# Kernel tuning notes

Measured on AMD Instinct MI355X. Metric: run time of the kernel, lower is better.

## Reference

```python
import jax, jax.numpy as jnp
import numpy as np

NU, NI, E, B, D = 100000, 50000, 1000000, 250000, 64
MSG_EPS = 1e-7   # GENConv message epsilon
BN_EPS = 1e-5    # BatchNorm1d epsilon


def setup_inputs() -> dict:
    key = jax.random.key(0)
    ks = jax.random.split(key, 8)
    x_user = jax.random.normal(ks[0], (NU, D), jnp.float32)
    x_item = jax.random.normal(ks[1], (NI, D), jnp.float32)
    src_u = jax.random.randint(ks[2], (E,), 0, NU)
    dst_i = jax.random.randint(ks[3], (E,), 0, NI)
    edge_ui = jnp.stack([src_u, dst_i]).astype(jnp.int32)   # (user, rates, item)
    pu = jax.random.randint(ks[4], (B,), 0, NU)
    pi = jax.random.randint(ks[5], (B,), 0, NI)
    pred_edge = jnp.stack([pu, pi]).astype(jnp.int32)       # supervision edges
    # per-layer (3), per-edge-type (2: 0 = user->item conv, 1 = item->user conv)
    W1 = jax.random.normal(ks[6], (3, 2, D, 2 * D), jnp.float32) / np.sqrt(D).astype(np.float32)
    b1 = jnp.zeros((3, 2, 2 * D), jnp.float32)
    gamma = jnp.ones((3, 2, 2 * D), jnp.float32)
    beta = jnp.zeros((3, 2, 2 * D), jnp.float32)
    W2 = jax.random.normal(ks[7], (3, 2, 2 * D, D), jnp.float32) / np.sqrt(2 * D).astype(np.float32)
    b2 = jnp.zeros((3, 2, D), jnp.float32)
    return dict(x_user=x_user, x_item=x_item, W1=W1, b1=b1, gamma=gamma,
                beta=beta, W2=W2, b2=b2, edge_ui=edge_ui, pred_edge=pred_edge)


def _genconv(x_src, x_dst, src_idx, dst_idx, n_dst, W1, b1, g, bt, W2, b2):
    # message: relu(x_j) + eps   (no edge attrs)
    m = jax.nn.relu(x_src[src_idx]) + MSG_EPS                     # [E, D]
    # softmax aggregation over incoming edges per destination (t = 1)
    mx = jax.ops.segment_max(m, dst_idx, num_segments=n_dst)      # [N_dst, D]
    ex = jnp.exp(m - mx[dst_idx])
    den = jax.ops.segment_sum(ex, dst_idx, num_segments=n_dst)
    w = ex / den[dst_idx]
    agg = jax.ops.segment_sum(w * m, dst_idx, num_segments=n_dst) # [N_dst, D]
    # root skip + MLP([D, 2D, D]) with BatchNorm + ReLU on hidden layer
    h = agg + x_dst
    h = h @ W1 + b1                                               # [N_dst, 2D]
    mu = h.mean(axis=0)
    var = h.var(axis=0)
    h = g * (h - mu) * jax.lax.rsqrt(var + BN_EPS) + bt
    h = jax.nn.relu(h)
    return h @ W2 + b2                                            # [N_dst, D]


def reference(x_user, x_item, W1, b1, gamma, beta, W2, b2, edge_ui, pred_edge):
    u_idx, i_idx = edge_ui[0], edge_ui[1]
    xu, xi = x_user, x_item
    for l in range(3):
        # to_hetero: one conv per edge type; aggr='sum' trivial (one edge type per dst)
        new_i = _genconv(xu, xi, u_idx, i_idx, NI,
                         W1[l, 0], b1[l, 0], gamma[l, 0], beta[l, 0], W2[l, 0], b2[l, 0])
        new_u = _genconv(xi, xu, i_idx, u_idx, NU,
                         W1[l, 1], b1[l, 1], gamma[l, 1], beta[l, 1], W2[l, 1], b2[l, 1])
        xu = jax.nn.relu(new_u)
        xi = jax.nn.relu(new_i)
    # decoder: dot product on supervision edges
    return (xu[pred_edge[0]] * xi[pred_edge[1]]).sum(axis=-1)     # [B]
```

## Files before the change

### kernel.cpp

```cpp
#include <hip/hip_runtime.h>
#include <hip/hip_fp16.h>

#define NUSR 100000
#define NITM 50000
#define NEDG 1000000
#define NPRED 250000
#define DD 64
#define DD2 128
#define MSG_EPS 1e-7f
#define BN_EPS 1e-5f
#define SCAN_B 1024
#define LOG2E 1.44269504088896340736f
#define LN2F 0.69314718055994530942f

#define KI 98
#define KU 98
#define EPB 4096
#define ICAP 1536

typedef _Float16 f16x8 __attribute__((ext_vector_type(8)));
typedef float f32x4 __attribute__((ext_vector_type(4)));


__device__ __forceinline__ float exp2a(float x) {
    float r; asm("v_exp_f32 %0, %1" : "=v"(r) : "v"(x)); return r;
}

__global__ __launch_bounds__(256) void count_k(
    const int* __restrict__ u_idx, const int* __restrict__ i_idx,
    int* __restrict__ deg_u, int* __restrict__ deg_i)
{
    int base = (blockIdx.x * 256 + threadIdx.x) * 4;
    int u[4], it[4];
    #pragma unroll
    for (int q = 0; q < 4; q++) {
        int e = base + q;
        u[q]  = (e < NEDG) ? u_idx[e] : -1;
        it[q] = (e < NEDG) ? i_idx[e] : -1;
    }
    #pragma unroll
    for (int q = 0; q < 4; q++) if (it[q] >= 0) atomicAdd(&deg_i[it[q]], 1);
    #pragma unroll
    for (int q = 0; q < 4; q++) if (u[q] >= 0) atomicAdd(&deg_u[u[q]], 1);
}

__global__ __launch_bounds__(SCAN_B) void scan1_k(
    const int* __restrict__ deg_i, const int* __restrict__ deg_u,
    int* __restrict__ part_i, int* __restrict__ part_u,
    int* __restrict__ bsum_i, int* __restrict__ bsum_u, int nbi)
{
    __shared__ int s[SCAN_B];
    const int* deg; int* partial; int* bsum; int n, bb;
    if ((int)blockIdx.x < nbi) { deg = deg_i; partial = part_i; bsum = bsum_i; n = NITM; bb = blockIdx.x; }
    else { deg = deg_u; partial = part_u; bsum = bsum_u; n = NUSR; bb = blockIdx.x - nbi; }
    int tid = threadIdx.x;
    int i = bb * SCAN_B + tid;
    s[tid] = (i < n) ? deg[i] : 0;
    __syncthreads();
    for (int off = 1; off < SCAN_B; off <<= 1) {
        int t = (tid >= off) ? s[tid - off] : 0;
        __syncthreads();
        s[tid] += t;
        __syncthreads();
    }
    if (i < n) partial[i] = s[tid];
    if (tid == SCAN_B - 1) bsum[bb] = s[tid];
}

__global__ __launch_bounds__(128) void scan2_k(
    int* __restrict__ bsum_i, int* __restrict__ bsum_u, int nbi, int nbu)
{
    __shared__ int s[128];
    int* bsum = (blockIdx.x == 0) ? bsum_i : bsum_u;
    int nb = (blockIdx.x == 0) ? nbi : nbu;
    int tid = threadIdx.x;
    s[tid] = (tid < nb) ? bsum[tid] : 0;
    __syncthreads();
    for (int off = 1; off < 128; off <<= 1) {
        int t = (tid >= off) ? s[tid - off] : 0;
        __syncthreads();
        s[tid] += t;
        __syncthreads();
    }
    if (tid < nb) bsum[tid] = (tid == 0) ? 0 : s[tid - 1];
}

__global__ __launch_bounds__(SCAN_B) void scan3_k(
    const int* __restrict__ deg_i, const int* __restrict__ deg_u,
    const int* __restrict__ part_i, const int* __restrict__ part_u,
    const int* __restrict__ bsum_i, const int* __restrict__ bsum_u,
    int* __restrict__ rowptr_i, int* __restrict__ rowptr_u,
    int* __restrict__ bcur_i, int* __restrict__ bcur_u, int nbi)
{
    const int* deg; const int* partial; const int* bsum;
    int* rowptr; int* bcur; int n, bb, sh;
    if ((int)blockIdx.x < nbi) {
        deg = deg_i; partial = part_i; bsum = bsum_i;
        rowptr = rowptr_i; bcur = bcur_i; n = NITM; bb = blockIdx.x; sh = 9;
    } else {
        deg = deg_u; partial = part_u; bsum = bsum_u;
        rowptr = rowptr_u; bcur = bcur_u; n = NUSR; bb = blockIdx.x - nbi; sh = 10;
    }
    int i = bb * SCAN_B + threadIdx.x;
    if (i < n) {
        int rs = partial[i] - deg[i] + bsum[bb];
        rowptr[i] = rs;
        if ((i & ((1 << sh) - 1)) == 0) bcur[i >> sh] = rs;
    }
    if (i == 0) rowptr[n] = NEDG;
}

__global__ __launch_bounds__(256) void part_k(
    const int* __restrict__ u_idx, const int* __restrict__ i_idx,
    int* __restrict__ bcur_i, int* __restrict__ bcur_u,
    int* __restrict__ pair_i, int* __restrict__ pair_u)
{
    __shared__ int lh_i[KI], lh_u[KU];
    __shared__ int lb_i[KI], lb_u[KU];
    int tid = threadIdx.x;
    int base = blockIdx.x * EPB;
    int u[16], it[16];
    #pragma unroll
    for (int q = 0; q < 16; q++) {
        int e = base + q * 256 + tid;
        u[q]  = (e < NEDG) ? u_idx[e] : -1;
        it[q] = (e < NEDG) ? i_idx[e] : -1;
    }
    if (tid < KI) lh_i[tid] = 0;
    if (tid >= 128 && tid < 128 + KU) lh_u[tid - 128] = 0;
    __syncthreads();
    #pragma unroll
    for (int q = 0; q < 16; q++) if (it[q] >= 0) {
        atomicAdd(&lh_i[it[q] >> 9], 1);
        atomicAdd(&lh_u[u[q] >> 10], 1);
    }
    __syncthreads();
    if (tid < KI) { int c = lh_i[tid]; lb_i[tid] = c ? atomicAdd(&bcur_i[tid], c) : 0; }
    if (tid >= 128 && tid < 128 + KU) {
        int k = tid - 128; int c = lh_u[k];
        lb_u[k] = c ? atomicAdd(&bcur_u[k], c) : 0;
    }
    __syncthreads();
    #pragma unroll
    for (int q = 0; q < 16; q++) if (it[q] >= 0) {
        int pi_ = atomicAdd(&lb_i[it[q] >> 9], 1);
        pair_i[pi_] = ((it[q] & 511) << 17) | u[q];
        int pu_ = atomicAdd(&lb_u[u[q] >> 10], 1);
        pair_u[pu_] = ((u[q] & 1023) << 16) | it[q];
    }
}

__global__ __launch_bounds__(1024) void bscat_k(
    const int* __restrict__ pair_i, const int* __restrict__ pair_u,
    const int* __restrict__ rowptr_i, const int* __restrict__ rowptr_u,
    int* __restrict__ csr_i, int* __restrict__ csr_u)
{
    __shared__ int cur[1024];
    int b = blockIdx.x;
    const int* pair; const int* rowptr; int* csr;
    int base_row, wrows, n, shsrc;
    if (b < KI) {
        pair = pair_i; rowptr = rowptr_i; csr = csr_i;
        base_row = b << 9; wrows = 512; n = NITM; shsrc = 17;
    } else {
        int k = b - KI;
        pair = pair_u; rowptr = rowptr_u; csr = csr_u;
        base_row = k << 10; wrows = 1024; n = NUSR; shsrc = 16;
    }
    int nrows = min(wrows, n - base_row);
    int t = threadIdx.x;
    if (t < nrows) cur[t] = rowptr[base_row + t];
    __syncthreads();
    int bstart = rowptr[base_row];
    int bend = rowptr[min(base_row + wrows, n)];
    int srcmask = (1 << shsrc) - 1;
    for (int e = bstart + t; e < bend; e += 1024) {
        int v = pair[e];
        int pos = atomicAdd(&cur[v >> shsrc], 1);
        csr[pos] = v & srcmask;
    }
}

__global__ __launch_bounds__(256) void msg0_k(
    const float* __restrict__ xu, const float* __restrict__ xi,
    __half* __restrict__ ef_u, __half* __restrict__ ef_i,
    __half* __restrict__ xh_u, __half* __restrict__ xh_i)
{
    int i = blockIdx.x * 256 + threadIdx.x;
    const float* x; __half* ef; __half* xh; int idx;
    if (i < NUSR * 16) { x = xu; ef = ef_u; xh = xh_u; idx = i; }
    else { int j = i - NUSR * 16; if (j >= NITM * 16) return; x = xi; ef = ef_i; xh = xh_i; idx = j; }
    float4 v = ((const float4*)x)[idx];
    float m0 = (fmaxf(v.x, 0.f) + MSG_EPS) * LOG2E;
    float m1 = (fmaxf(v.y, 0.f) + MSG_EPS) * LOG2E;
    float m2 = (fmaxf(v.z, 0.f) + MSG_EPS) * LOG2E;
    float m3 = (fmaxf(v.w, 0.f) + MSG_EPS) * LOG2E;
    __half2 e01 = __floats2half2_rn(m0, m1), e23 = __floats2half2_rn(m2, m3);
    __half2 x01 = __floats2half2_rn(v.x, v.y), x23 = __floats2half2_rn(v.z, v.w);
    uint2 ew, xw;
    ew.x = *(unsigned int*)&e01; ew.y = *(unsigned int*)&e23;
    xw.x = *(unsigned int*)&x01; xw.y = *(unsigned int*)&x23;
    ((uint2*)ef)[idx] = ew;
    ((uint2*)xh)[idx] = xw;
}

__global__ __launch_bounds__(256) void wconv_k(
    const float* __restrict__ W1, const float* __restrict__ W2,
    __half* __restrict__ W1t, __half* __restrict__ W2t)
{
    int idx = blockIdx.x * 256 + threadIdx.x;
    if (idx >= 6 * 8192) return;
    int m = idx >> 13, rem = idx & 8191;
    {
        int k = rem >> 7, c = rem & 127;
        W1t[m * 8192 + c * 64 + k] = __float2half(W1[idx]);
    }
    {
        int k = rem >> 6, c = rem & 63;
        W2t[m * 8192 + c * 128 + k] = __float2half(W2[idx]);
    }
}

#define UPD4(U) { \
    float2 va=__half22float2(*(__half2*)&(U).x); \
    float2 vb=__half22float2(*(__half2*)&(U).y); \
    float2 vc=__half22float2(*(__half2*)&(U).z); \
    float2 vd=__half22float2(*(__half2*)&(U).w); \
    float e0=exp2a(va.x), e1=exp2a(va.y), e2=exp2a(vb.x), e3=exp2a(vb.y); \
    float e4=exp2a(vc.x), e5=exp2a(vc.y), e6=exp2a(vd.x), e7=exp2a(vd.y); \
    d0+=e0; n0=fmaf(e0,va.x,n0); d1+=e1; n1=fmaf(e1,va.y,n1); \
    d2+=e2; n2=fmaf(e2,vb.x,n2); d3+=e3; n3=fmaf(e3,vb.y,n3); \
    d4+=e4; n4=fmaf(e4,vc.x,n4); d5+=e5; n5=fmaf(e5,vc.y,n5); \
    d6+=e6; n6=fmaf(e6,vd.x,n6); d7+=e7; n7=fmaf(e7,vd.y,n7); }

#define GBODY(IDXE) { \
    int j = beg; \
    for (; j + 8 <= end; j += 8) { \
        int s0=(IDXE(j)),   s1=(IDXE(j+1)), s2=(IDXE(j+2)), s3=(IDXE(j+3)); \
        int s4=(IDXE(j+4)), s5=(IDXE(j+5)), s6=(IDXE(j+6)), s7=(IDXE(j+7)); \
        uint4 u0 = mp4[(size_t)s0*8+l8]; uint4 u1 = mp4[(size_t)s1*8+l8]; \
        uint4 u2 = mp4[(size_t)s2*8+l8]; uint4 u3 = mp4[(size_t)s3*8+l8]; \
        uint4 u4 = mp4[(size_t)s4*8+l8]; uint4 u5 = mp4[(size_t)s5*8+l8]; \
        uint4 u6 = mp4[(size_t)s6*8+l8]; uint4 u7 = mp4[(size_t)s7*8+l8]; \
        UPD4(u0) UPD4(u1) UPD4(u2) UPD4(u3) UPD4(u4) UPD4(u5) UPD4(u6) UPD4(u7) } \
    for (; j + 2 <= end; j += 2) { \
        int s0=(IDXE(j)), s1=(IDXE(j+1)); \
        uint4 u0 = mp4[(size_t)s0*8+l8]; uint4 u1 = mp4[(size_t)s1*8+l8]; \
        UPD4(u0) UPD4(u1) } \
    if (j < end) { int ss=(IDXE(j)); uint4 uu = mp4[(size_t)ss*8+l8]; UPD4(uu) } }

#define IDX_L(jj) su.idx[(jj)]
#define IDX_G(jj) csr[blkBeg + (jj)]

union AggSU { int idx[ICAP]; float red[8][128]; };

__global__ __launch_bounds__(256) void aggemm1f_k(
    const __half* __restrict__ ef_i_src, const __half* __restrict__ ef_u_src,
    const __half* __restrict__ xhi_cur, const __half* __restrict__ xhu_cur,
    const int* __restrict__ rowptr_i, const int* __restrict__ rowptr_u,
    const int* __restrict__ csr_i, const int* __restrict__ csr_u,
    const __half* __restrict__ W1t_l,
    const float* __restrict__ b1_l,
    __half* __restrict__ h1_i, __half* __restrict__ h1_u,
    double* __restrict__ gs_l,
    int gI)
{
    __shared__ _Float16 sA[64][88];
    __shared__ AggSU su;
    __shared__ int srp[65];
    __shared__ int wq;

    int side = ((int)blockIdx.x < gI) ? 0 : 1;
    int bb = side ? (blockIdx.x - gI) : blockIdx.x;
    const __half* ef  = side ? ef_i_src : ef_u_src;
    const __half* xh  = side ? xhu_cur : xhi_cur;
    const int* rowptr = side ? rowptr_u : rowptr_i;
    const int* csr    = side ? csr_u : csr_i;
    const __half* W1t = W1t_l + (size_t)side * 8192;
    const float* b1   = b1_l + side * DD2;
    __half* h1        = side ? h1_u : h1_i;
    double* gsum      = gs_l + side * 256;
    double* gsq       = gsum + 128;
    int N             = side ? NUSR : NITM;

    int t = threadIdx.x;
    int r0 = bb * 64;
    int w = t >> 6, lane = t & 63;
    int g = lane >> 3, l8 = lane & 7;
    int q = lane >> 4, ln = lane & 15;
    const uint4* mp4 = (const uint4*)ef;

    int blkBeg = rowptr[r0];
    if (t == 0) wq = 0;
    if (t < 65) srp[t] = rowptr[min(r0 + t, N)] - blkBeg;
    int blkEnd = rowptr[min(r0 + 64, N)];
    int nE = blkEnd - blkBeg;
    for (int e = t; e < nE && e < ICAP; e += 256) su.idx[e] = csr[blkBeg + e];
    __syncthreads();

    for (;;) {
        int rr = 0;
        if (l8 == 0) rr = atomicAdd(&wq, 1);
        rr = __shfl(rr, g * 8);
        if (rr >= 64) break;
        int r = r0 + rr;
        uint4 o = make_uint4(0u, 0u, 0u, 0u);
        if (r < N) {
            uint4 xv = ((const uint4*)xh)[(size_t)r * 8 + l8];
            int beg = srp[rr], end = srp[rr + 1];
            float d0=0.f,d1=0.f,d2=0.f,d3=0.f,d4=0.f,d5=0.f,d6=0.f,d7=0.f;
            float n0=0.f,n1=0.f,n2=0.f,n3=0.f,n4=0.f,n5=0.f,n6=0.f,n7=0.f;
            if (end <= ICAP) { GBODY(IDX_L) } else { GBODY(IDX_G) }
            bool nz = end > beg;
            float a0 = nz ? (n0/d0)*LN2F : 0.f, a1 = nz ? (n1/d1)*LN2F : 0.f;
            float a2 = nz ? (n2/d2)*LN2F : 0.f, a3 = nz ? (n3/d3)*LN2F : 0.f;
            float a4 = nz ? (n4/d4)*LN2F : 0.f, a5 = nz ? (n5/d5)*LN2F : 0.f;
            float a6 = nz ? (n6/d6)*LN2F : 0.f, a7 = nz ? (n7/d7)*LN2F : 0.f;
            float2 x01 = __half22float2(*(__half2*)&xv.x);
            float2 x23 = __half22float2(*(__half2*)&xv.y);
            float2 x45 = __half22float2(*(__half2*)&xv.z);
            float2 x67 = __half22float2(*(__half2*)&xv.w);
            __half2 p0 = __floats2half2_rn(a0 + x01.x, a1 + x01.y);
            __half2 p1 = __floats2half2_rn(a2 + x23.x, a3 + x23.y);
            __half2 p2 = __floats2half2_rn(a4 + x45.x, a5 + x45.y);
            __half2 p3 = __floats2half2_rn(a6 + x67.x, a7 + x67.y);
            o.x = *(unsigned int*)&p0; o.y = *(unsigned int*)&p1;
            o.z = *(unsigned int*)&p2; o.w = *(unsigned int*)&p3;
        }
        *(uint4*)&sA[rr][l8 * 8] = o;
    }
    __syncthreads();

    f16x8 afr[4][2], bfr[2][2];
    #pragma unroll
    for (int rt = 0; rt < 4; rt++)
        #pragma unroll
        for (int ks = 0; ks < 2; ks++)
            afr[rt][ks] = *(const f16x8*)&sA[rt * 16 + ln][ks * 32 + q * 8];
    const f16x8* Wv = (const f16x8*)W1t;
    #pragma unroll
    for (int ct = 0; ct < 2; ct++)
        #pragma unroll
        for (int ks = 0; ks < 2; ks++)
            bfr[ct][ks] = Wv[(w * 32 + ct * 16 + ln) * 8 + ks * 4 + q];

    f32x4 acc[4][2];
    #pragma unroll
    for (int rt = 0; rt < 4; rt++)
        #pragma unroll
        for (int ct = 0; ct < 2; ct++)
            acc[rt][ct] = (f32x4){0.f, 0.f, 0.f, 0.f};

    #pragma unroll
    for (int rt = 0; rt < 4; rt++)
        #pragma unroll
        for (int ct = 0; ct < 2; ct++) {
            acc[rt][ct] = __builtin_amdgcn_mfma_f32_16x16x32_f16(
                afr[rt][0], bfr[ct][0], acc[rt][ct], 0, 0, 0);
            acc[rt][ct] = __builtin_amdgcn_mfma_f32_16x16x32_f16(
                afr[rt][1], bfr[ct][1], acc[rt][ct], 0, 0, 0);
        }

    float b1c0 = b1[w * 32 + ln];
    float b1c1 = b1[w * 32 + 16 + ln];
    float ps0 = 0.f, pq0 = 0.f, ps1 = 0.f, pq1 = 0.f;
    #pragma unroll
    for (int rt = 0; rt < 4; rt++) {
        #pragma unroll
        for (int i = 0; i < 4; i++) {
            int r = r0 + rt * 16 + q * 4 + i;
            if (r < N) {
                float h0 = acc[rt][0][i] + b1c0;
                float h1v = acc[rt][1][i] + b1c1;
                h1[(size_t)r * DD2 + w * 32 + ln] = __float2half(h0);
                h1[(size_t)r * DD2 + w * 32 + 16 + ln] = __float2half(h1v);
                ps0 += h0; pq0 += h0 * h0;
                ps1 += h1v; pq1 += h1v * h1v;
            }
        }
    }
    su.red[q][w * 32 + ln] = ps0;      su.red[q][w * 32 + 16 + ln] = ps1;
    su.red[4 + q][w * 32 + ln] = pq0;  su.red[4 + q][w * 32 + 16 + ln] = pq1;
    __syncthreads();
    if (t < 128) {
        float s = 0.f, qq = 0.f;
        #pragma unroll
        for (int k = 0; k < 4; k++) { s += su.red[k][t]; qq += su.red[4 + k][t]; }
        atomicAdd(&gsum[t], (double)s);
        atomicAdd(&gsq[t],  (double)qq);
    }
}

__global__ __launch_bounds__(256) void gemm2f_k(
    const __half* __restrict__ h1_i, const __half* __restrict__ h1_u,
    const double* __restrict__ gs_l,
    const float* __restrict__ gamma_l, const float* __restrict__ beta_l,
    const __half* __restrict__ W2t_l, const float* __restrict__ b2_l,
    float* __restrict__ xi_new, float* __restrict__ xu_new,
    __half* __restrict__ xhi_out, __half* __restrict__ xhu_out,
    __half* __restrict__ efi_out, __half* __restrict__ efu_out,
    int last, int gI)
{
    __shared__ _Float16 sA[64][136];
    __shared__ float2 sss[DD2];

    int side = ((int)blockIdx.x < gI) ? 0 : 1;
    int bb = side ? (blockIdx.x - gI) : blockIdx.x;
    const __half* h1   = side ? h1_u : h1_i;
    const double* gsum = gs_l + side * 256;
    const double* gsq  = gsum + 128;
    const float* gamma = gamma_l + side * DD2;
    const float* beta  = beta_l + side * DD2;
    const __half* W2t  = W2t_l + (size_t)side * 8192;
    const float* b2    = b2_l + side * DD;
    float* xnew        = side ? xu_new : xi_new;
    __half* xhout      = side ? xhu_out : xhi_out;
    __half* efout      = side ? efu_out : efi_out;
    int N              = side ? NUSR : NITM;

    int t = threadIdx.x;
    if (t < 128) {
        double mean = gsum[t] / (double)N;
        double var  = gsq[t] / (double)N - mean * mean;
        float inv = (float)(1.0 / sqrt(var + (double)BN_EPS));
        float sc = gamma[t] * inv;
        sss[t] = make_float2(sc, beta[t] - (float)mean * sc);
    }
    __syncthreads();

    int r0 = bb * 64;
    for (int i = t; i < 2048; i += 256) {
        int rr = i >> 5, c4 = i & 31;
        int r = r0 + rr;
        uint2 o = make_uint2(0u, 0u);
        if (r < N) {
            uint2 hv = ((const uint2*)h1)[(size_t)r * 32 + c4];
            float2 va = __half22float2(*(__half2*)&hv.x);
            float2 vb = __half22float2(*(__half2*)&hv.y);
            float2 s0 = sss[c4 * 4], s1 = sss[c4 * 4 + 1];
            float2 s2 = sss[c4 * 4 + 2], s3 = sss[c4 * 4 + 3];
            va.x = fmaxf(fmaf(va.x, s0.x, s0.y), 0.f);
            va.y = fmaxf(fmaf(va.y, s1.x, s1.y), 0.f);
            vb.x = fmaxf(fmaf(vb.x, s2.x, s2.y), 0.f);
            vb.y = fmaxf(fmaf(vb.y, s3.x, s3.y), 0.f);
            __half2 a = __floats2half2_rn(va.x, va.y);
            __half2 b = __floats2half2_rn(vb.x, vb.y);
            o.x = *(unsigned int*)&a; o.y = *(unsigned int*)&b;
        }
        *(uint2*)&sA[rr][c4 * 4] = o;
    }
    __syncthreads();

    int w = t >> 6, lane = t & 63, q = lane >> 4, ln = lane & 15;
    f32x4 acc[4];
    #pragma unroll
    for (int rt = 0; rt < 4; rt++) acc[rt] = (f32x4){0.f, 0.f, 0.f, 0.f};

    const f16x8* Wv = (const f16x8*)W2t;
    #pragma unroll
    for (int ks = 0; ks < 4; ks++) {
        f16x8 bf = Wv[(w * 16 + ln) * 16 + ks * 4 + q];
        #pragma unroll
        for (int rt = 0; rt < 4; rt++) {
            f16x8 af = *(const f16x8*)&sA[rt * 16 + ln][ks * 32 + q * 8];
            acc[rt] = __builtin_amdgcn_mfma_f32_16x16x32_f16(af, bf, acc[rt], 0, 0, 0);
        }
    }

    int c = w * 16 + ln;
    float bb2 = b2[c];
    #pragma unroll
    for (int rt = 0; rt < 4; rt++) {
        #pragma unroll
        for (int i = 0; i < 4; i++) {
            int r = r0 + rt * 16 + q * 4 + i;
            if (r < N) {
                float o = fmaxf(acc[rt][i] + bb2, 0.f);
                if (last) {
                    xnew[(size_t)r * DD + c] = o;
                } else {
                    xhout[(size_t)r * DD + c] = __float2half(o);
                    efout[(size_t)r * DD + c] = __float2half((o + MSG_EPS) * LOG2E);
                }
            }
        }
    }
}

__global__ __launch_bounds__(256) void decode_k(
    const float* __restrict__ xu, const float* __restrict__ xi,
    const int* __restrict__ pu, const int* __restrict__ pi,
    float* __restrict__ out)
{
    int idx = blockIdx.x * 256 + threadIdx.x;
    int b = idx >> 4, lane = idx & 15;
    if (b >= NPRED) return;
    int u = pu[b], it = pi[b];
    float4 a = ((const float4*)(xu + (size_t)u * DD))[lane];
    float4 c = ((const float4*)(xi + (size_t)it * DD))[lane];
    float s = a.x * c.x + a.y * c.y + a.z * c.z + a.w * c.w;
    #pragma unroll
    for (int off = 8; off; off >>= 1) s += __shfl_down(s, off, 16);
    if (lane == 0) out[b] = s;
}

extern "C" void kernel_launch(void* const* d_in, const int* in_sizes, int n_in,
                              void* d_out, int out_size, void* d_ws, size_t ws_size,
                              hipStream_t stream)
{
    const float* x_user = (const float*)d_in[0];
    const float* x_item = (const float*)d_in[1];
    const float* W1    = (const float*)d_in[2];
    const float* b1    = (const float*)d_in[3];
    const float* gamma = (const float*)d_in[4];
    const float* beta  = (const float*)d_in[5];
    const float* W2    = (const float*)d_in[6];
    const float* b2    = (const float*)d_in[7];
    const int* edge = (const int*)d_in[8];
    const int* pred = (const int*)d_in[9];
    float* out = (float*)d_out;

    const int* u_idx = edge;
    const int* i_idx = edge + NEDG;

    char* p = (char*)d_ws;
    #define ALLOC(ptr, type, count) \
        type* ptr = (type*)p; p += (((size_t)(count) * sizeof(type)) + 255) & ~(size_t)255;

    ALLOC(deg_i, int, NITM)
    ALLOC(deg_u, int, NUSR)
    ALLOC(gsumAll, double, 12 * 256)
    size_t zero_span = (char*)p - (char*)deg_i;
    ALLOC(part_i, int, NITM)
    ALLOC(part_u, int, NUSR)
    ALLOC(bsum_i, int, 128)
    ALLOC(bsum_u, int, 128)
    ALLOC(bcur_i, int, 128)
    ALLOC(bcur_u, int, 128)
    ALLOC(rowptr_i, int, NITM + 1)
    ALLOC(rowptr_u, int, NUSR + 1)
    ALLOC(csr_i, int, NEDG)
    ALLOC(csr_u, int, NEDG)
    ALLOC(h1_i, __half, (size_t)NITM * DD2)
    ALLOC(h1_u, __half, (size_t)NUSR * DD2)
    ALLOC(W1t, __half, 6 * 8192)
    ALLOC(W2t, __half, 6 * 8192)
    ALLOC(xu_f, float, (size_t)NUSR * DD)
    ALLOC(xi_f, float, (size_t)NITM * DD)
    ALLOC(xh_u0, __half, (size_t)NUSR * DD)
    ALLOC(xh_u1, __half, (size_t)NUSR * DD)
    ALLOC(xh_i0, __half, (size_t)NITM * DD)
    ALLOC(xh_i1, __half, (size_t)NITM * DD)
    ALLOC(ef_u, __half, (size_t)NUSR * DD)
    ALLOC(ef_i0, __half, (size_t)NITM * DD)
    ALLOC(ef_i1, __half, (size_t)NITM * DD)
    #undef ALLOC

    int* pair_i = (int*)h1_i;
    int* pair_u = (int*)h1_u;

    hipMemsetAsync(deg_i, 0, zero_span, stream);
    int eb4 = (NEDG / 4 + 255) / 256;
    count_k<<<eb4, 256, 0, stream>>>(u_idx, i_idx, deg_u, deg_i);

    int nbi = (NITM + SCAN_B - 1) / SCAN_B;
    int nbu = (NUSR + SCAN_B - 1) / SCAN_B;
    scan1_k<<<nbi + nbu, SCAN_B, 0, stream>>>(deg_i, deg_u, part_i, part_u,
                                              bsum_i, bsum_u, nbi);
    scan2_k<<<2, 128, 0, stream>>>(bsum_i, bsum_u, nbi, nbu);
    scan3_k<<<nbi + nbu, SCAN_B, 0, stream>>>(deg_i, deg_u, part_i, part_u,
                                              bsum_i, bsum_u, rowptr_i, rowptr_u,
                                              bcur_i, bcur_u, nbi);
    int pb = (NEDG + EPB - 1) / EPB;
    part_k<<<pb, 256, 0, stream>>>(u_idx, i_idx, bcur_i, bcur_u, pair_i, pair_u);
    bscat_k<<<KI + KU, 1024, 0, stream>>>(pair_i, pair_u, rowptr_i, rowptr_u,
                                          csr_i, csr_u);

    wconv_k<<<(6 * 8192 + 255) / 256, 256, 0, stream>>>(W1, W2, W1t, W2t);
    msg0_k<<<((NUSR + NITM) * 16 + 255) / 256, 256, 0, stream>>>(
        x_user, x_item, ef_u, ef_i0, xh_u0, xh_i0);

    int gI = (NITM + 63) / 64;
    int gU = (NUSR + 63) / 64;
    __half* efi = ef_i0;
    __half* efi_alt = ef_i1;
    for (int l = 0; l < 3; l++) {
        const __half* xhi_c = (l & 1) ? xh_i1 : xh_i0;
        const __half* xhu_c = (l & 1) ? xh_u1 : xh_u0;
        __half* xhi_o = (l & 1) ? xh_i0 : xh_i1;
        __half* xhu_o = (l & 1) ? xh_u0 : xh_u1;
        aggemm1f_k<<<gI + gU, 256, 0, stream>>>(
            efi, ef_u, xhi_c, xhu_c, rowptr_i, rowptr_u, csr_i, csr_u,
            W1t + (size_t)l * 2 * 8192, b1 + (size_t)l * 2 * DD2,
            h1_i, h1_u, gsumAll + l * 2 * 256, gI);
        gemm2f_k<<<gI + gU, 256, 0, stream>>>(
            h1_i, h1_u, gsumAll + l * 2 * 256,
            gamma + (size_t)l * 2 * DD2, beta + (size_t)l * 2 * DD2,
            W2t + (size_t)l * 2 * 8192, b2 + (size_t)l * 2 * DD,
            xi_f, xu_f, xhi_o, xhu_o, efi_alt, ef_u, (l == 2) ? 1 : 0, gI);
        __half* tmp = efi; efi = efi_alt; efi_alt = tmp;
    }

    decode_k<<<(NPRED * 16) / 256, 256, 0, stream>>>(xu_f, xi_f, pred, pred + NPRED, out);
}
```

Measured before the change: 557.8 us.

## Store aggregated input and recompute first GEMM instead of storing hidden activations

The fused aggregate+GEMM1 kernel is split into three kernels. An aggregation kernel writes the 64-wide fp16 aggregated input. A stats kernel recomputes GEMM1 only to accumulate the BatchNorm sums. The MLP kernel recomputes GEMM1, then applies BN+ReLU in shared memory and runs GEMM2. This avoids writing and re-reading the 128-wide hidden tensor, at the cost of computing GEMM1 twice and one extra launch per layer. The aggregation kernel also uses less shared memory, which may raise occupancy.

Measured after the change: 624.3 us. 11.9% more time.

```diff
diff --git a/kernel.cpp b/kernel.cpp
--- a/kernel.cpp
+++ b/kernel.cpp
@@ -249,24 +249,17 @@
         UPD4(u0) UPD4(u1) } \
     if (j < end) { int ss=(IDXE(j)); uint4 uu = mp4[(size_t)ss*8+l8]; UPD4(uu) } }
 
-#define IDX_L(jj) su.idx[(jj)]
+#define IDX_L(jj) sidx[(jj)]
 #define IDX_G(jj) csr[blkBeg + (jj)]
 
-union AggSU { int idx[ICAP]; float red[8][128]; };
-
-__global__ __launch_bounds__(256) void aggemm1f_k(
+__global__ __launch_bounds__(256) void agg_k(
     const __half* __restrict__ ef_i_src, const __half* __restrict__ ef_u_src,
     const __half* __restrict__ xhi_cur, const __half* __restrict__ xhu_cur,
     const int* __restrict__ rowptr_i, const int* __restrict__ rowptr_u,
     const int* __restrict__ csr_i, const int* __restrict__ csr_u,
-    const __half* __restrict__ W1t_l,
-    const float* __restrict__ b1_l,
-    __half* __restrict__ h1_i, __half* __restrict__ h1_u,
-    double* __restrict__ gs_l,
-    int gI)
-{
-    __shared__ _Float16 sA[64][88];
-    __shared__ AggSU su;
+    __half* __restrict__ p_i, __half* __restrict__ p_u, int gI)
+{
+    __shared__ int sidx[ICAP];
     __shared__ int srp[65];
     __shared__ int wq;
 
@@ -276,18 +269,13 @@
     const __half* xh  = side ? xhu_cur : xhi_cur;
     const int* rowptr = side ? rowptr_u : rowptr_i;
     const int* csr    = side ? csr_u : csr_i;
-    const __half* W1t = W1t_l + (size_t)side * 8192;
-    const float* b1   = b1_l + side * DD2;
-    __half* h1        = side ? h1_u : h1_i;
-    double* gsum      = gs_l + side * 256;
-    double* gsq       = gsum + 128;
+    __half* pd        = side ? p_u : p_i;
     int N             = side ? NUSR : NITM;
 
     int t = threadIdx.x;
     int r0 = bb * 64;
-    int w = t >> 6, lane = t & 63;
+    int lane = t & 63;
     int g = lane >> 3, l8 = lane & 7;
-    int q = lane >> 4, ln = lane & 15;
     const uint4* mp4 = (const uint4*)ef;
 
     int blkBeg = rowptr[r0];
@@ -295,7 +283,7 @@
     if (t < 65) srp[t] = rowptr[min(r0 + t, N)] - blkBeg;
     int blkEnd = rowptr[min(r0 + 64, N)];
     int nE = blkEnd - blkBeg;
-    for (int e = t; e < nE && e < ICAP; e += 256) su.idx[e] = csr[blkBeg + e];
+    for (int e = t; e < nE && e < ICAP; e += 256) sidx[e] = csr[blkBeg + e];
     __syncthreads();
 
     for (;;) {
@@ -327,17 +315,36 @@
             o.x = *(unsigned int*)&p0; o.y = *(unsigned int*)&p1;
             o.z = *(unsigned int*)&p2; o.w = *(unsigned int*)&p3;
         }
-        *(uint4*)&sA[rr][l8 * 8] = o;
-    }
-    __syncthreads();
+        ((uint4*)pd)[(size_t)(r0 + rr) * 8 + l8] = o;
+    }
+}
+
+__global__ __launch_bounds__(256) void stat_k(
+    const __half* __restrict__ p_i, const __half* __restrict__ p_u,
+    const __half* __restrict__ W1t_l, const float* __restrict__ b1_l,
+    double* __restrict__ gs_l, int gI)
+{
+    __shared__ float red[8][128];
+
+    int side = ((int)blockIdx.x < gI) ? 0 : 1;
+    int bb = side ? (blockIdx.x - gI) : blockIdx.x;
+    const f16x8* pv = (const f16x8*)(side ? p_u : p_i);
+    const f16x8* Wv = (const f16x8*)(W1t_l + (size_t)side * 8192);
+    const float* b1 = b1_l + side * DD2;
+    double* gsum    = gs_l + side * 256;
+    double* gsq     = gsum + 128;
+    int N           = side ? NUSR : NITM;
+
+    int t = threadIdx.x;
+    int r0 = bb * 64;
+    int w = t >> 6, lane = t & 63, q = lane >> 4, ln = lane & 15;
 
     f16x8 afr[4][2], bfr[2][2];
     #pragma unroll
     for (int rt = 0; rt < 4; rt++)
         #pragma unroll
         for (int ks = 0; ks < 2; ks++)
-            afr[rt][ks] = *(const f16x8*)&sA[rt * 16 + ln][ks * 32 + q * 8];
-    const f16x8* Wv = (const f16x8*)W1t;
+            afr[rt][ks] = pv[(size_t)(r0 + rt * 16 + ln) * 8 + ks * 4 + q];
     #pragma unroll
     for (int ct = 0; ct < 2; ct++)
         #pragma unroll
@@ -350,7 +357,6 @@
         #pragma unroll
         for (int ct = 0; ct < 2; ct++)
             acc[rt][ct] = (f32x4){0.f, 0.f, 0.f, 0.f};
-
     #pragma unroll
     for (int rt = 0; rt < 4; rt++)
         #pragma unroll
@@ -372,46 +378,47 @@
             if (r < N) {
                 float h0 = acc[rt][0][i] + b1c0;
                 float h1v = acc[rt][1][i] + b1c1;
-                h1[(size_t)r * DD2 + w * 32 + ln] = __float2half(h0);
-                h1[(size_t)r * DD2 + w * 32 + 16 + ln] = __float2half(h1v);
                 ps0 += h0; pq0 += h0 * h0;
                 ps1 += h1v; pq1 += h1v * h1v;
             }
         }
     }
-    su.red[q][w * 32 + ln] = ps0;      su.red[q][w * 32 + 16 + ln] = ps1;
-    su.red[4 + q][w * 32 + ln] = pq0;  su.red[4 + q][w * 32 + 16 + ln] = pq1;
+    red[q][w * 32 + ln] = ps0;      red[q][w * 32 + 16 + ln] = ps1;
+    red[4 + q][w * 32 + ln] = pq0;  red[4 + q][w * 32 + 16 + ln] = pq1;
     __syncthreads();
     if (t < 128) {
         float s = 0.f, qq = 0.f;
         #pragma unroll
-        for (int k = 0; k < 4; k++) { s += su.red[k][t]; qq += su.red[4 + k][t]; }
+        for (int k = 0; k < 4; k++) { s += red[k][t]; qq += red[4 + k][t]; }
         atomicAdd(&gsum[t], (double)s);
         atomicAdd(&gsq[t],  (double)qq);
     }
 }
 
-__global__ __launch_bounds__(256) void gemm2f_k(
-    const __half* __restrict__ h1_i, const __half* __restrict__ h1_u,
+__global__ __launch_bounds__(256) void mlp_k(
+    const __half* __restrict__ p_i, const __half* __restrict__ p_u,
     const double* __restrict__ gs_l,
     const float* __restrict__ gamma_l, const float* __restrict__ beta_l,
+    const __half* __restrict__ W1t_l, const float* __restrict__ b1_l,
     const __half* __restrict__ W2t_l, const float* __restrict__ b2_l,
     float* __restrict__ xi_new, float* __restrict__ xu_new,
     __half* __restrict__ xhi_out, __half* __restrict__ xhu_out,
     __half* __restrict__ efi_out, __half* __restrict__ efu_out,
     int last, int gI)
 {
-    __shared__ _Float16 sA[64][136];
+    __shared__ _Float16 sH[64][136];
     __shared__ float2 sss[DD2];
 
     int side = ((int)blockIdx.x < gI) ? 0 : 1;
     int bb = side ? (blockIdx.x - gI) : blockIdx.x;
-    const __half* h1   = side ? h1_u : h1_i;
+    const f16x8* pv    = (const f16x8*)(side ? p_u : p_i);
     const double* gsum = gs_l + side * 256;
     const double* gsq  = gsum + 128;
     const float* gamma = gamma_l + side * DD2;
     const float* beta  = beta_l + side * DD2;
-    const __half* W2t  = W2t_l + (size_t)side * 8192;
+    const f16x8* W1v   = (const f16x8*)(W1t_l + (size_t)side * 8192);
+    const float* b1    = b1_l + side * DD2;
+    const f16x8* W2v   = (const f16x8*)(W2t_l + (size_t)side * 8192);
     const float* b2    = b2_l + side * DD;
     float* xnew        = side ? xu_new : xi_new;
     __half* xhout      = side ? xhu_out : xhi_out;
@@ -419,6 +426,9 @@
     int N              = side ? NUSR : NITM;
 
     int t = threadIdx.x;
+    int r0 = bb * 64;
+    int w = t >> 6, lane = t & 63, q = lane >> 4, ln = lane & 15;
+
     if (t < 128) {
         double mean = gsum[t] / (double)N;
         double var  = gsq[t] / (double)N - mean * mean;
@@ -426,44 +436,62 @@
         float sc = gamma[t] * inv;
         sss[t] = make_float2(sc, beta[t] - (float)mean * sc);
     }
-    __syncthreads();
-
-    int r0 = bb * 64;
-    for (int i = t; i < 2048; i += 256) {
-        int rr = i >> 5, c4 = i & 31;
-        int r = r0 + rr;
-        uint2 o = make_uint2(0u, 0u);
-        if (r < N) {
-            uint2 hv = ((const uint2*)h1)[(size_t)r * 32 + c4];
-            float2 va = __half22float2(*(__half2*)&hv.x);
-            float2 vb = __half22float2(*(__half2*)&hv.y);
-            float2 s0 = sss[c4 * 4], s1 = sss[c4 * 4 + 1];
-            float2 s2 = sss[c4 * 4 + 2], s3 = sss[c4 * 4 + 3];
-            va.x = fmaxf(fmaf(va.x, s0.x, s0.y), 0.f);
-            va.y = fmaxf(fmaf(va.y, s1.x, s1.y), 0.f);
-            vb.x = fmaxf(fmaf(vb.x, s2.x, s2.y), 0.f);
-            vb.y = fmaxf(fmaf(vb.y, s3.x, s3.y), 0.f);
-            __half2 a = __floats2half2_rn(va.x, va.y);
-            __half2 b = __floats2half2_rn(vb.x, vb.y);
-            o.x = *(unsigned int*)&a; o.y = *(unsigned int*)&b;
+
+    f16x8 afr[4][2], bfr[2][2];
+    #pragma unroll
+    for (int rt = 0; rt < 4; rt++)
+        #pragma unroll
+        for (int ks = 0; ks < 2; ks++)
+            afr[rt][ks] = pv[(size_t)(r0 + rt * 16 + ln) * 8 + ks * 4 + q];
+    #pragma unroll
+    for (int ct = 0; ct < 2; ct++)
+        #pragma unroll
+        for (int ks = 0; ks < 2; ks++)
+            bfr[ct][ks] = W1v[(w * 32 + ct * 16 + ln) * 8 + ks * 4 + q];
+
+    f32x4 acc[4][2];
+    #pragma unroll
+    for (int rt = 0; rt < 4; rt++)
+        #pragma unroll
+        for (int ct = 0; ct < 2; ct++)
+            acc[rt][ct] = (f32x4){0.f, 0.f, 0.f, 0.f};
+    #pragma unroll
+    for (int rt = 0; rt < 4; rt++)
+        #pragma unroll
+        for (int ct = 0; ct < 2; ct++) {
+            acc[rt][ct] = __builtin_amdgcn_mfma_f32_16x16x32_f16(
+                afr[rt][0], bfr[ct][0], acc[rt][ct], 0, 0, 0);
+            acc[rt][ct] = __builtin_amdgcn_mfma_f32_16x16x32_f16(
+                afr[rt][1], bfr[ct][1], acc[rt][ct], 0, 0, 0);
         }
-        *(uint2*)&sA[rr][c4 * 4] = o;
-    }
-    __syncthreads();
-
-    int w = t >> 6, lane = t & 63, q = lane >> 4, ln = lane & 15;
-    f32x4 acc[4];
-    #pragma unroll
-    for (int rt = 0; rt < 4; rt++) acc[rt] = (f32x4){0.f, 0.f, 0.f, 0.f};
-
-    const f16x8* Wv = (const f16x8*)W2t;
+    __syncthreads();
+
+    int c0 = w * 32 + ln, c1 = c0 + 16;
+    float b1c0 = b1[c0], b1c1 = b1[c1];
+    float2 s0 = sss[c0], s1 = sss[c1];
+    #pragma unroll
+    for (int rt = 0; rt < 4; rt++) {
+        #pragma unroll
+        for (int i = 0; i < 4; i++) {
+            int row = rt * 16 + q * 4 + i;
+            float h0 = acc[rt][0][i] + b1c0;
+            float h1v = acc[rt][1][i] + b1c1;
+            sH[row][c0] = (_Float16)fmaxf(fmaf(h0, s0.x, s0.y), 0.f);
+            sH[row][c1] = (_Float16)fmaxf(fmaf(h1v, s1.x, s1.y), 0.f);
+        }
+    }
+    __syncthreads();
+
+    f32x4 acc2[4];
+    #pragma unroll
+    for (int rt = 0; rt < 4; rt++) acc2[rt] = (f32x4){0.f, 0.f, 0.f, 0.f};
     #pragma unroll
     for (int ks = 0; ks < 4; ks++) {
-        f16x8 bf = Wv[(w * 16 + ln) * 16 + ks * 4 + q];
+        f16x8 bf = W2v[(w * 16 + ln) * 16 + ks * 4 + q];
         #pragma unroll
         for (int rt = 0; rt < 4; rt++) {
-            f16x8 af = *(const f16x8*)&sA[rt * 16 + ln][ks * 32 + q * 8];
-            acc[rt] = __builtin_amdgcn_mfma_f32_16x16x32_f16(af, bf, acc[rt], 0, 0, 0);
+            f16x8 af = *(const f16x8*)&sH[rt * 16 + ln][ks * 32 + q * 8];
+            acc2[rt] = __builtin_amdgcn_mfma_f32_16x16x32_f16(af, bf, acc2[rt], 0, 0, 0);
         }
     }
 
@@ -475,7 +503,7 @@
         for (int i = 0; i < 4; i++) {
             int r = r0 + rt * 16 + q * 4 + i;
             if (r < N) {
-                float o = fmaxf(acc[rt][i] + bb2, 0.f);
+                float o = fmaxf(acc2[rt][i] + bb2, 0.f);
                 if (last) {
                     xnew[(size_t)r * DD + c] = o;
                 } else {
@@ -541,8 +569,8 @@
     ALLOC(rowptr_u, int, NUSR + 1)
     ALLOC(csr_i, int, NEDG)
     ALLOC(csr_u, int, NEDG)
-    ALLOC(h1_i, __half, (size_t)NITM * DD2)
-    ALLOC(h1_u, __half, (size_t)NUSR * DD2)
+    ALLOC(p_i, __half, (size_t)(NITM + 64) * DD)
+    ALLOC(p_u, __half, (size_t)(NUSR + 64) * DD)
     ALLOC(W1t, __half, 6 * 8192)
     ALLOC(W2t, __half, 6 * 8192)
     ALLOC(xu_f, float, (size_t)NUSR * DD)
@@ -556,8 +584,8 @@
     ALLOC(ef_i1, __half, (size_t)NITM * DD)
     #undef ALLOC
 
-    int* pair_i = (int*)h1_i;
-    int* pair_u = (int*)h1_u;
+    int* pair_i = (int*)p_i;
+    int* pair_u = (int*)p_u;
 
     hipMemsetAsync(deg_i, 0, zero_span, stream);
     int eb4 = (NEDG / 4 + 255) / 256;
@@ -589,13 +617,16 @@
         const __half* xhu_c = (l & 1) ? xh_u1 : xh_u0;
         __half* xhi_o = (l & 1) ? xh_i0 : xh_i1;
         __half* xhu_o = (l & 1) ? xh_u0 : xh_u1;
-        aggemm1f_k<<<gI + gU, 256, 0, stream>>>(
+        agg_k<<<gI + gU, 256, 0, stream>>>(
             efi, ef_u, xhi_c, xhu_c, rowptr_i, rowptr_u, csr_i, csr_u,
+            p_i, p_u, gI);
+        stat_k<<<gI + gU, 256, 0, stream>>>(
+            p_i, p_u, W1t + (size_t)l * 2 * 8192, b1 + (size_t)l * 2 * DD2,
+            gsumAll + l * 2 * 256, gI);
+        mlp_k<<<gI + gU, 256, 0, stream>>>(
+            p_i, p_u, gsumAll + l * 2 * 256,
+            gamma + (size_t)l * 2 * DD2, beta + (size_t)l * 2 * DD2,
             W1t + (size_t)l * 2 * 8192, b1 + (size_t)l * 2 * DD2,
-            h1_i, h1_u, gsumAll + l * 2 * 256, gI);
-        gemm2f_k<<<gI + gU, 256, 0, stream>>>(
-            h1_i, h1_u, gsumAll + l * 2 * 256,
-            gamma + (size_t)l * 2 * DD2, beta + (size_t)l * 2 * DD2,
             W2t + (size_t)l * 2 * 8192, b2 + (size_t)l * 2 * DD,
             xi_f, xu_f, xhi_o, xhu_o, efi_alt, ef_u, (l == 2) ? 1 : 0, gI);
         __half* tmp = efi; efi = efi_alt; efi_alt = tmp;
```

## Build CSR via fixed-capacity buckets with in-block degree histograms and scans

Applied to the files above, without the earlier changes.

Removes the global degree-count atomics pass and the three-kernel global prefix scan. Edges are now partitioned directly into fixed-capacity per-bucket regions. Each scatter block then builds the degree histogram for its rows in shared memory, scans it locally, and writes rowptr using a tiny bucket-base scan. This cuts three kernel launches and a full pass over the edge list with global atomics. The risk is a bucket overflowing BCAP (16384) if the degree distribution were skewed, and pair buffers are reused in the h1 storage at a larger footprint.

After: 475.6 us. -14.7%, faster.

```diff
diff --git a/kernel.cpp b/kernel.cpp
--- a/kernel.cpp
+++ b/kernel.cpp
@@ -9,12 +9,12 @@
 #define DD2 128
 #define MSG_EPS 1e-7f
 #define BN_EPS 1e-5f
-#define SCAN_B 1024
 #define LOG2E 1.44269504088896340736f
 #define LN2F 0.69314718055994530942f
 
 #define KI 98
 #define KU 98
+#define BCAP 16384
 #define EPB 4096
 #define ICAP 1536
 
@@ -26,93 +26,9 @@
     float r; asm("v_exp_f32 %0, %1" : "=v"(r) : "v"(x)); return r;
 }
 
-__global__ __launch_bounds__(256) void count_k(
-    const int* __restrict__ u_idx, const int* __restrict__ i_idx,
-    int* __restrict__ deg_u, int* __restrict__ deg_i)
-{
-    int base = (blockIdx.x * 256 + threadIdx.x) * 4;
-    int u[4], it[4];
-    #pragma unroll
-    for (int q = 0; q < 4; q++) {
-        int e = base + q;
-        u[q]  = (e < NEDG) ? u_idx[e] : -1;
-        it[q] = (e < NEDG) ? i_idx[e] : -1;
-    }
-    #pragma unroll
-    for (int q = 0; q < 4; q++) if (it[q] >= 0) atomicAdd(&deg_i[it[q]], 1);
-    #pragma unroll
-    for (int q = 0; q < 4; q++) if (u[q] >= 0) atomicAdd(&deg_u[u[q]], 1);
-}
-
-__global__ __launch_bounds__(SCAN_B) void scan1_k(
-    const int* __restrict__ deg_i, const int* __restrict__ deg_u,
-    int* __restrict__ part_i, int* __restrict__ part_u,
-    int* __restrict__ bsum_i, int* __restrict__ bsum_u, int nbi)
-{
-    __shared__ int s[SCAN_B];
-    const int* deg; int* partial; int* bsum; int n, bb;
-    if ((int)blockIdx.x < nbi) { deg = deg_i; partial = part_i; bsum = bsum_i; n = NITM; bb = blockIdx.x; }
-    else { deg = deg_u; partial = part_u; bsum = bsum_u; n = NUSR; bb = blockIdx.x - nbi; }
-    int tid = threadIdx.x;
-    int i = bb * SCAN_B + tid;
-    s[tid] = (i < n) ? deg[i] : 0;
-    __syncthreads();
-    for (int off = 1; off < SCAN_B; off <<= 1) {
-        int t = (tid >= off) ? s[tid - off] : 0;
-        __syncthreads();
-        s[tid] += t;
-        __syncthreads();
-    }
-    if (i < n) partial[i] = s[tid];
-    if (tid == SCAN_B - 1) bsum[bb] = s[tid];
-}
-
-__global__ __launch_bounds__(128) void scan2_k(
-    int* __restrict__ bsum_i, int* __restrict__ bsum_u, int nbi, int nbu)
-{
-    __shared__ int s[128];
-    int* bsum = (blockIdx.x == 0) ? bsum_i : bsum_u;
-    int nb = (blockIdx.x == 0) ? nbi : nbu;
-    int tid = threadIdx.x;
-    s[tid] = (tid < nb) ? bsum[tid] : 0;
-    __syncthreads();
-    for (int off = 1; off < 128; off <<= 1) {
-        int t = (tid >= off) ? s[tid - off] : 0;
-        __syncthreads();
-        s[tid] += t;
-        __syncthreads();
-    }
-    if (tid < nb) bsum[tid] = (tid == 0) ? 0 : s[tid - 1];
-}
-
-__global__ __launch_bounds__(SCAN_B) void scan3_k(
-    const int* __restrict__ deg_i, const int* __restrict__ deg_u,
-    const int* __restrict__ part_i, const int* __restrict__ part_u,
-    const int* __restrict__ bsum_i, const int* __restrict__ bsum_u,
-    int* __restrict__ rowptr_i, int* __restrict__ rowptr_u,
-    int* __restrict__ bcur_i, int* __restrict__ bcur_u, int nbi)
-{
-    const int* deg; const int* partial; const int* bsum;
-    int* rowptr; int* bcur; int n, bb, sh;
-    if ((int)blockIdx.x < nbi) {
-        deg = deg_i; partial = part_i; bsum = bsum_i;
-        rowptr = rowptr_i; bcur = bcur_i; n = NITM; bb = blockIdx.x; sh = 9;
-    } else {
-        deg = deg_u; partial = part_u; bsum = bsum_u;
-        rowptr = rowptr_u; bcur = bcur_u; n = NUSR; bb = blockIdx.x - nbi; sh = 10;
-    }
-    int i = bb * SCAN_B + threadIdx.x;
-    if (i < n) {
-        int rs = partial[i] - deg[i] + bsum[bb];
-        rowptr[i] = rs;
-        if ((i & ((1 << sh) - 1)) == 0) bcur[i >> sh] = rs;
-    }
-    if (i == 0) rowptr[n] = NEDG;
-}
-
 __global__ __launch_bounds__(256) void part_k(
     const int* __restrict__ u_idx, const int* __restrict__ i_idx,
-    int* __restrict__ bcur_i, int* __restrict__ bcur_u,
+    int* __restrict__ bkcnt_i, int* __restrict__ bkcnt_u,
     int* __restrict__ pair_i, int* __restrict__ pair_u)
 {
     __shared__ int lh_i[KI], lh_u[KU];
@@ -135,10 +51,13 @@
         atomicAdd(&lh_u[u[q] >> 10], 1);
     }
     __syncthreads();
-    if (tid < KI) { int c = lh_i[tid]; lb_i[tid] = c ? atomicAdd(&bcur_i[tid], c) : 0; }
+    if (tid < KI) {
+        int c = lh_i[tid];
+        lb_i[tid] = tid * BCAP + (c ? atomicAdd(&bkcnt_i[tid], c) : 0);
+    }
     if (tid >= 128 && tid < 128 + KU) {
         int k = tid - 128; int c = lh_u[k];
-        lb_u[k] = c ? atomicAdd(&bcur_u[k], c) : 0;
+        lb_u[k] = k * BCAP + (c ? atomicAdd(&bkcnt_u[k], c) : 0);
     }
     __syncthreads();
     #pragma unroll
@@ -150,31 +69,67 @@
     }
 }
 
-__global__ __launch_bounds__(1024) void bscat_k(
+__global__ __launch_bounds__(128) void bsum2_k(
+    const int* __restrict__ bkcnt_i, const int* __restrict__ bkcnt_u,
+    int* __restrict__ bbase_i, int* __restrict__ bbase_u)
+{
+    __shared__ int s[128];
+    const int* cnt = (blockIdx.x == 0) ? bkcnt_i : bkcnt_u;
+    int* bas = (blockIdx.x == 0) ? bbase_i : bbase_u;
+    int t = threadIdx.x;
+    int v = (t < KI) ? cnt[t] : 0;
+    s[t] = v;
+    __syncthreads();
+    for (int off = 1; off < 128; off <<= 1) {
+        int tv = (t >= off) ? s[t - off] : 0;
+        __syncthreads();
+        s[t] += tv;
+        __syncthreads();
+    }
+    if (t < KI) bas[t] = s[t] - v;
+}
+
+__global__ __launch_bounds__(1024) void bscat2_k(
     const int* __restrict__ pair_i, const int* __restrict__ pair_u,
-    const int* __restrict__ rowptr_i, const int* __restrict__ rowptr_u,
+    const int* __restrict__ bkcnt_i, const int* __restrict__ bkcnt_u,
+    const int* __restrict__ bbase_i, const int* __restrict__ bbase_u,
+    int* __restrict__ rowptr_i, int* __restrict__ rowptr_u,
     int* __restrict__ csr_i, int* __restrict__ csr_u)
 {
+    __shared__ int s[1024];
     __shared__ int cur[1024];
     int b = blockIdx.x;
-    const int* pair; const int* rowptr; int* csr;
-    int base_row, wrows, n, shsrc;
+    const int* pair; int* rowptr; int* csr;
+    int base_row, wrows, n, shsrc, cnt, base;
     if (b < KI) {
-        pair = pair_i; rowptr = rowptr_i; csr = csr_i;
-        base_row = b << 9; wrows = 512; n = NITM; shsrc = 17;
+        pair = pair_i + (size_t)b * BCAP; cnt = bkcnt_i[b]; base = bbase_i[b];
+        rowptr = rowptr_i; csr = csr_i; base_row = b << 9; wrows = 512; n = NITM; shsrc = 17;
     } else {
         int k = b - KI;
-        pair = pair_u; rowptr = rowptr_u; csr = csr_u;
-        base_row = k << 10; wrows = 1024; n = NUSR; shsrc = 16;
+        pair = pair_u + (size_t)k * BCAP; cnt = bkcnt_u[k]; base = bbase_u[k];
+        rowptr = rowptr_u; csr = csr_u; base_row = k << 10; wrows = 1024; n = NUSR; shsrc = 16;
     }
     int nrows = min(wrows, n - base_row);
     int t = threadIdx.x;
-    if (t < nrows) cur[t] = rowptr[base_row + t];
-    __syncthreads();
-    int bstart = rowptr[base_row];
-    int bend = rowptr[min(base_row + wrows, n)];
+    s[t] = 0;
+    __syncthreads();
+    for (int e = t; e < cnt; e += 1024) atomicAdd(&s[pair[e] >> shsrc], 1);
+    __syncthreads();
+    int deg = s[t];
+    for (int off = 1; off < 1024; off <<= 1) {
+        int tv = (t >= off) ? s[t - off] : 0;
+        __syncthreads();
+        s[t] += tv;
+        __syncthreads();
+    }
+    int rp = base + s[t] - deg;
+    if (t < nrows) rowptr[base_row + t] = rp;
+    cur[t] = rp;
+    if (b == KI - 1 && t == 0) rowptr_i[NITM] = NEDG;
+    if (b == KI + KU - 1 && t == 0) rowptr_u[NUSR] = NEDG;
+    __syncthreads();
     int srcmask = (1 << shsrc) - 1;
-    for (int e = bstart + t; e < bend; e += 1024) {
+    for (int e = t; e < cnt; e += 1024) {
         int v = pair[e];
         int pos = atomicAdd(&cur[v >> shsrc], 1);
         csr[pos] = v & srcmask;
@@ -527,16 +482,12 @@
     #define ALLOC(ptr, type, count) \
         type* ptr = (type*)p; p += (((size_t)(count) * sizeof(type)) + 255) & ~(size_t)255;
 
-    ALLOC(deg_i, int, NITM)
-    ALLOC(deg_u, int, NUSR)
     ALLOC(gsumAll, double, 12 * 256)
-    size_t zero_span = (char*)p - (char*)deg_i;
-    ALLOC(part_i, int, NITM)
-    ALLOC(part_u, int, NUSR)
-    ALLOC(bsum_i, int, 128)
-    ALLOC(bsum_u, int, 128)
-    ALLOC(bcur_i, int, 128)
-    ALLOC(bcur_u, int, 128)
+    ALLOC(bkcnt_i, int, 128)
+    ALLOC(bkcnt_u, int, 128)
+    size_t zero_span = (char*)p - (char*)gsumAll;
+    ALLOC(bbase_i, int, 128)
+    ALLOC(bbase_u, int, 128)
     ALLOC(rowptr_i, int, NITM + 1)
     ALLOC(rowptr_u, int, NUSR + 1)
     ALLOC(csr_i, int, NEDG)
@@ -559,22 +510,13 @@
     int* pair_i = (int*)h1_i;
     int* pair_u = (int*)h1_u;
 
-    hipMemsetAsync(deg_i, 0, zero_span, stream);
-    int eb4 = (NEDG / 4 + 255) / 256;
-    count_k<<<eb4, 256, 0, stream>>>(u_idx, i_idx, deg_u, deg_i);
-
-    int nbi = (NITM + SCAN_B - 1) / SCAN_B;
-    int nbu = (NUSR + SCAN_B - 1) / SCAN_B;
-    scan1_k<<<nbi + nbu, SCAN_B, 0, stream>>>(deg_i, deg_u, part_i, part_u,
-                                              bsum_i, bsum_u, nbi);
-    scan2_k<<<2, 128, 0, stream>>>(bsum_i, bsum_u, nbi, nbu);
-    scan3_k<<<nbi + nbu, SCAN_B, 0, stream>>>(deg_i, deg_u, part_i, part_u,
-                                              bsum_i, bsum_u, rowptr_i, rowptr_u,
-                                              bcur_i, bcur_u, nbi);
+    hipMemsetAsync(gsumAll, 0, zero_span, stream);
     int pb = (NEDG + EPB - 1) / EPB;
-    part_k<<<pb, 256, 0, stream>>>(u_idx, i_idx, bcur_i, bcur_u, pair_i, pair_u);
-    bscat_k<<<KI + KU, 1024, 0, stream>>>(pair_i, pair_u, rowptr_i, rowptr_u,
-                                          csr_i, csr_u);
+    part_k<<<pb, 256, 0, stream>>>(u_idx, i_idx, bkcnt_i, bkcnt_u, pair_i, pair_u);
+    bsum2_k<<<2, 128, 0, stream>>>(bkcnt_i, bkcnt_u, bbase_i, bbase_u);
+    bscat2_k<<<KI + KU, 1024, 0, stream>>>(pair_i, pair_u, bkcnt_i, bkcnt_u,
+                                           bbase_i, bbase_u, rowptr_i, rowptr_u,
+                                           csr_i, csr_u);
 
     wconv_k<<<(6 * 8192 + 255) / 256, 256, 0, stream>>>(W1, W2, W1t, W2t);
     msg0_k<<<((NUSR + NITM) * 16 + 255) / 256, 256, 0, stream>>>(
```
